# Kernel tuning notes

Hardware: AMD Instinct MI355X
Metric: run time of the kernel (lower is better)

## Reference

```python
import jax, jax.numpy as jnp
import numpy as np
import math

B, N, E_PER = 128, 512, 2048
D = 16
NUM_REL = 114
NUM_ATTR = 10
LAYERS = 3
RATIO = 0.8
TN = B * N
TE = B * E_PER
NEG_SLOPE = 0.2


def setup_inputs() -> dict:
    key = jax.random.key(0)
    ks = jax.random.split(key, 16)
    x_attr = jax.random.randint(ks[0], (TN,), 0, NUM_ATTR, dtype=jnp.int32)
    # edges constrained within each graph's contiguous block of N nodes
    src = jax.random.randint(ks[1], (B, E_PER), 0, N, dtype=jnp.int32)
    dst = jax.random.randint(ks[2], (B, E_PER), 0, N, dtype=jnp.int32)
    off = (jnp.arange(B, dtype=jnp.int32) * N)[:, None]
    edge_index = jnp.stack([(src + off).reshape(-1), (dst + off).reshape(-1)])
    edge_type = jax.random.randint(ks[3], (TE,), 0, NUM_REL, dtype=jnp.int32)
    emb = jax.random.normal(ks[4], (NUM_ATTR, D)) * 0.3
    gnn_w = jax.random.normal(ks[5], (LAYERS, NUM_REL, D, D)) * (1.0 / np.sqrt(D))
    gnn_q = jax.random.normal(ks[6], (LAYERS, D, 1)) * 0.3
    gnn_k = jax.random.normal(ks[7], (LAYERS, D, 1)) * 0.3
    gnn_b = jnp.zeros((LAYERS, D))
    pool_w = jax.random.normal(ks[8], (LAYERS - 1, D)) * 0.3
    w1 = jax.random.normal(ks[9], (D * LAYERS * 2, 16)) * (1.0 / np.sqrt(D * LAYERS * 2))
    b1 = jnp.zeros((16,))
    w2 = jax.random.normal(ks[10], (16, 4)) * 0.25
    b2 = jnp.zeros((4,))
    w3 = jax.random.normal(ks[11], (4, 1)) * 0.5
    b3 = jnp.zeros((1,))
    return dict(emb=emb, gnn_w=gnn_w, gnn_q=gnn_q, gnn_k=gnn_k, gnn_b=gnn_b,
                pool_w=pool_w, w1=w1, b1=b1, w2=w2, b2=b2, w3=w3, b3=b3,
                x_attr=x_attr, edge_index=edge_index, edge_type=edge_type)


def _rgat_layer(x, src, dst, etype, edge_mask, node_mask, W, q, k, b):
    # PyG RGATConv: heads=1, dim=1, additive-self-attention, across-relation softmax, sum aggr
    w_e = W[etype]                                   # [E, D, D] per-relation gather
    h_s = jnp.einsum('ed,edo->eo', x[src], w_e)      # transformed source (x_j)
    h_t = jnp.einsum('ed,edo->eo', x[dst], w_e)      # transformed target (x_i)
    logit = jax.nn.leaky_relu((h_t @ q + h_s @ k)[:, 0], NEG_SLOPE)  # [E]
    # masked segment softmax over incoming edges of each target node
    m = jax.ops.segment_max(jnp.where(edge_mask, logit, -jnp.inf), dst, num_segments=TN)
    m_e = m[dst]
    ex = jnp.where(edge_mask, jnp.exp(logit - jnp.where(jnp.isfinite(m_e), m_e, 0.0)), 0.0)
    den = jax.ops.segment_sum(ex, dst, num_segments=TN)[dst]
    alpha = ex / jnp.where(den > 0, den, 1.0)
    out = jax.ops.segment_sum(alpha[:, None] * h_s, dst, num_segments=TN) + b
    return jnp.where(node_mask[:, None], jax.nn.relu(out), 0.0)


def reference(emb, gnn_w, gnn_q, gnn_k, gnn_b, pool_w, w1, b1, w2, b2, w3, b3,
              x_attr, edge_index, edge_type):
    src, dst = edge_index[0], edge_index[1]
    x = emb[x_attr]                                  # [TN, D]
    node_mask = jnp.ones((TN,), bool)
    edge_mask = jnp.ones((TE,), bool)
    feats = []
    alive = N
    for l in range(LAYERS):
        x = _rgat_layer(x, src, dst, edge_type, edge_mask, node_mask,
                        gnn_w[l], gnn_q[l], gnn_k[l], gnn_b[l])
        xb = x.reshape(B, N, D)
        mb = node_mask.reshape(B, N)
        cnt = mb.sum(1).astype(x.dtype)[:, None]
        feats.append(xb.sum(1) / cnt)                               # global mean pool
        feats.append(jnp.where(mb[:, :, None], xb, -jnp.inf).max(1))  # global max pool
        if l < LAYERS - 1:
            kk = math.ceil(RATIO * alive)            # static per-graph keep count
            pw = pool_w[l]
            score = jnp.tanh((x @ pw) / jnp.linalg.norm(pw))        # [TN]
            sm = jnp.where(node_mask, score, -jnp.inf).reshape(B, N)
            _, idx = jax.lax.top_k(sm, kk)
            nm = jnp.zeros((B, N), bool).at[jnp.arange(B)[:, None], idx].set(True).reshape(-1)
            x = jnp.where(nm[:, None], x * score[:, None], 0.0)
            node_mask = nm
            edge_mask = edge_mask & nm[src] & nm[dst]
            alive = kk
    g = jnp.concatenate(feats, axis=1)               # [B, 96]
    g = jax.nn.relu(g @ w1 + b1)
    g = jax.nn.relu(g @ w2 + b2)
    return jax.nn.sigmoid(g @ w3 + b3)               # [B, 1]
```

## Files before the change

### kernel.cpp

```cpp
#include <hip/hip_runtime.h>

#define B_ 128
#define NPG 512
#define EPG 2048
#define NREL 114
#define XS 18

__device__ __forceinline__ unsigned fkey(float f){
  unsigned u = __float_as_uint(f);
  return (u & 0x80000000u) ? ~u : (u | 0x80000000u);
}
__device__ __forceinline__ float fdec(unsigned k){
  return (k & 0x80000000u) ? __uint_as_float(k & 0x7FFFFFFFu) : __uint_as_float(~k);
}
__device__ __forceinline__ float dot4f(float4 a, float4 b){
  return a.x*b.x + a.y*b.y + a.z*b.z + a.w*b.w;
}

__device__ __forceinline__ void scan512(int* s_hist, int* s_off, int* s_wt, int tid){
  int lane = tid & 63, wv = tid >> 6;
  int cnt = 0, inc = 0;
  if (wv < 8){
    cnt = s_hist[wv*64 + lane];
    inc = cnt;
    #pragma unroll
    for (int o=1; o<64; o<<=1){ int t=__shfl_up(inc,o); if (lane>=o) inc += t; }
    if (lane==63) s_wt[wv] = inc;
  }
  __syncthreads();
  if (tid < 8){
    int e = 0;
    #pragma unroll
    for (int j=0;j<8;j++) if (j<tid) e += s_wt[j];
    s_wt[8+tid] = e;
  }
  __syncthreads();
  if (wv < 8){
    int base = s_wt[8+wv];
    s_off[wv*64+lane+1] = base + inc;
    s_hist[wv*64+lane]  = base + inc - cnt;
  }
  if (tid==0) s_off[0] = 0;
}

__global__ __launch_bounds__(1024) void k_fused(
    const float* __restrict__ emb, const float* __restrict__ gnn_w,
    const float* __restrict__ gnn_q, const float* __restrict__ gnn_k,
    const float* __restrict__ gnn_b, const float* __restrict__ pool_w,
    const float* __restrict__ w1, const float* __restrict__ b1,
    const float* __restrict__ w2, const float* __restrict__ b2,
    const float* __restrict__ w3, const float* __restrict__ b3,
    const int* __restrict__ xattr, const int* __restrict__ src,
    const int* __restrict__ dst, const int* __restrict__ et,
    float* __restrict__ out)
{
  __shared__ float s_x[NPG*XS];
  __shared__ float s_wq[NREL*XS];
  __shared__ float s_wk[NREL*XS];
  __shared__ float s_logit[EPG];
  __shared__ int s_off[NPG+1];
  __shared__ int s_hist[NPG];
  __shared__ unsigned s_keys[NPG];
  __shared__ int s_mask[NPG];
  __shared__ unsigned short s_esrc[EPG], s_edst[EPG], s_eet[EPG];
  __shared__ unsigned short s_perm[NPG];
  __shared__ int s_dh[64];
  __shared__ int s_wt[16];
  __shared__ float s_sum[16];
  __shared__ unsigned s_max16[16];
  __shared__ int s_w[16];
  __shared__ float s_feats[96];
  __shared__ float s_h1[16], s_h2[4];

  const int b = blockIdx.x, tid = threadIdx.x;
  const int lane = tid & 63, wv = tid >> 6;
  const int og = tid & 3, grp = tid >> 2;
  const int nb = b*NPG;
  const size_t gb = (size_t)b*EPG;

  if (tid < NPG){
    int a = xattr[nb + tid];
    const float2* e2 = (const float2*)(emb + a*16);
    #pragma unroll
    for (int c=0;c<8;c++) *(float2*)&s_x[tid*XS + 2*c] = e2[c];
    s_mask[tid] = 1;
  }
  for (int i=tid;i<NPG;i+=1024) s_hist[i]=0;
  if (tid<64) s_dh[tid]=0;
  __syncthreads();
  for (int e=tid;e<EPG;e+=1024) atomicAdd(&s_hist[dst[gb+e]-nb], 1);
  __syncthreads();
  scan512(s_hist, s_off, s_wt, tid);
  __syncthreads();
  {
    for (int e=tid;e<EPG;e+=1024){
      int d = dst[gb+e]-nb;
      int p = atomicAdd(&s_hist[d], 1);
      s_esrc[p] = (unsigned short)(src[gb+e]-nb);
      s_edst[p] = (unsigned short)d;
      s_eet[p]  = (unsigned short)et[gb+e];
    }
    int mydeg = 0;
    if (tid<NPG){
      mydeg = s_off[tid+1]-s_off[tid]; if (mydeg>63) mydeg=63;
      atomicAdd(&s_dh[mydeg], 1);
    }
    __syncthreads();
    if (tid<64){
      int c = s_dh[tid], inc = c;
      #pragma unroll
      for (int o=1;o<64;o<<=1){ int t=__shfl_up(inc,o); if (tid>=o) inc+=t; }
      s_dh[tid] = inc - c;
    }
    __syncthreads();
    if (tid<NPG){ int p = atomicAdd(&s_dh[mydeg],1); s_perm[p]=(unsigned short)tid; }
  }
  __syncthreads();

  const int cnts[3] = {512, 410, 328};
  const int kks[2]  = {410, 328};

  for (int l=0; l<3; ++l){
    const float* Wl = gnn_w + (size_t)l*NREL*256;
    {
      const float4* q4=(const float4*)(gnn_q+l*16);
      const float4* k4=(const float4*)(gnn_k+l*16);
      float4 q0=q4[0],q1=q4[1],q2=q4[2],q3=q4[3];
      float4 c0=k4[0],c1=k4[1],c2=k4[2],c3=k4[3];
      for (int i=tid;i<NREL*16;i+=1024){
        const float4* wr=(const float4*)(Wl+(size_t)i*16);
        float4 a0=wr[0],a1=wr[1],a2=wr[2],a3=wr[3];
        s_wq[(i>>4)*XS+(i&15)] = dot4f(a0,q0)+dot4f(a1,q1)+dot4f(a2,q2)+dot4f(a3,q3);
        s_wk[(i>>4)*XS+(i&15)] = dot4f(a0,c0)+dot4f(a1,c1)+dot4f(a2,c2)+dot4f(a3,c3);
      }
      if (tid<16){ s_sum[tid]=0.f; s_max16[tid]=0u; }
    }
    __syncthreads();
    float rnorm=0.f; float pw4[4]={0,0,0,0};
    if (l<2){
      float ss=0.f;
      #pragma unroll
      for (int o=0;o<16;o++){ float p=pool_w[l*16+o]; ss+=p*p; }
      rnorm = rsqrtf(ss);
      #pragma unroll
      for (int j=0;j<4;j++) pw4[j]=pool_w[l*16+4*og+j];
    }
    const float* bb = gnn_b + l*16;
    const int nA = s_perm[grp], nB = s_perm[511-grp];
    float zA[4], zB[4];
    auto pm_round = [&](int n, float* z){
      int beg = s_off[n], end = s_off[n+1];
      int alive = s_mask[n];
      float2 xt0 = *(const float2*)&s_x[n*XS+4*og];
      float2 xt1 = *(const float2*)&s_x[n*XS+4*og+2];
      float m = -1e30f;
      for (int p=beg; p<end; ++p){
        int s = s_esrc[p]; int r = s_eet[p];
        float2 wq0=*(const float2*)&s_wq[r*XS+4*og];
        float2 wq1=*(const float2*)&s_wq[r*XS+4*og+2];
        float2 wk0=*(const float2*)&s_wk[r*XS+4*og];
        float2 wk1=*(const float2*)&s_wk[r*XS+4*og+2];
        float2 xs0=*(const float2*)&s_x[s*XS+4*og];
        float2 xs1=*(const float2*)&s_x[s*XS+4*og+2];
        float a = xt0.x*wq0.x + xt0.y*wq0.y + xt1.x*wq1.x + xt1.y*wq1.y
                + xs0.x*wk0.x + xs0.y*wk0.y + xs1.x*wk1.x + xs1.y*wk1.y;
        a += __shfl_xor(a,1); a += __shfl_xor(a,2);
        float lg = a>0.f ? a : 0.2f*a;
        if (og==0) s_logit[p] = lg;
        m = fmaxf(m, lg);
      }
      float den=0.f, v0=0.f, v1=0.f, v2=0.f, v3=0.f;
      int p = beg;
      for (; p+2 <= end; p += 2){
        int s0=s_esrc[p],   r0=s_eet[p];
        int s1=s_esrc[p+1], r1=s_eet[p+1];
        float ex0 = __expf(s_logit[p]   - m);
        float ex1 = __expf(s_logit[p+1] - m);
        const float4* wr0 = (const float4*)(Wl + (size_t)r0*256) + og;
        const float4* wr1 = (const float4*)(Wl + (size_t)r1*256) + og;
        const float* xr0 = &s_x[s0*XS];
        const float* xr1 = &s_x[s1*XS];
        float h00=0.f,h01=0.f,h02=0.f,h03=0.f;
        float h10=0.f,h11=0.f,h12=0.f,h13=0.f;
        #pragma unroll
        for (int d2=0; d2<8; ++d2){
          float2 xa = *(const float2*)&xr0[2*d2];
          float2 xb = *(const float2*)&xr1[2*d2];
          float4 wA0 = wr0[(2*d2)*4], wB0 = wr0[(2*d2+1)*4];
          float4 wA1 = wr1[(2*d2)*4], wB1 = wr1[(2*d2+1)*4];
          h00 += xa.x*wA0.x + xa.y*wB0.x;  h01 += xa.x*wA0.y + xa.y*wB0.y;
          h02 += xa.x*wA0.z + xa.y*wB0.z;  h03 += xa.x*wA0.w + xa.y*wB0.w;
          h10 += xb.x*wA1.x + xb.y*wB1.x;  h11 += xb.x*wA1.y + xb.y*wB1.y;
          h12 += xb.x*wA1.z + xb.y*wB1.z;  h13 += xb.x*wA1.w + xb.y*wB1.w;
        }
        den += ex0 + ex1;
        v0 += ex0*h00 + ex1*h10; v1 += ex0*h01 + ex1*h11;
        v2 += ex0*h02 + ex1*h12; v3 += ex0*h03 + ex1*h13;
      }
      if (p < end){
        int s = s_esrc[p]; int r = s_eet[p];
        float ex = __expf(s_logit[p] - m);
        const float4* wr = (const float4*)(Wl + (size_t)r*256) + og;
        const float* xr = &s_x[s*XS];
        float h0=0.f,h1=0.f,h2=0.f,h3=0.f;
        #pragma unroll
        for (int d2=0; d2<8; ++d2){
          float2 xs2 = *(const float2*)&xr[2*d2];
          float4 wA = wr[(2*d2)*4];
          float4 wB = wr[(2*d2+1)*4];
          h0 += xs2.x*wA.x + xs2.y*wB.x;
          h1 += xs2.x*wA.y + xs2.y*wB.y;
          h2 += xs2.x*wA.z + xs2.y*wB.z;
          h3 += xs2.x*wA.w + xs2.y*wB.w;
        }
        den += ex;
        v0 += ex*h0; v1 += ex*h1; v2 += ex*h2; v3 += ex*h3;
      }
      float inv = den>0.f ? 1.f/den : 1.f;
      z[0]=v0*inv+bb[4*og+0]; z[1]=v1*inv+bb[4*og+1];
      z[2]=v2*inv+bb[4*og+2]; z[3]=v3*inv+bb[4*og+3];
      #pragma unroll
      for (int j=0;j<4;j++){ if (z[j]<0.f) z[j]=0.f; }
      if (!alive){ z[0]=z[1]=z[2]=z[3]=0.f; }
      #pragma unroll
      for (int j=0;j<4;j++){
        float sv=z[j], mv=z[j];
        #pragma unroll
        for (int off=4; off<64; off<<=1){
          sv += __shfl_xor(sv, off);
          mv = fmaxf(mv, __shfl_xor(mv, off));
        }
        if ((lane>>2)==0){
          atomicAdd(&s_sum[4*og+j], sv);
          atomicMax(&s_max16[4*og+j], __float_as_uint(mv));
        }
      }
      if (l<2){
        float dq = z[0]*pw4[0]+z[1]*pw4[1]+z[2]*pw4[2]+z[3]*pw4[3];
        dq += __shfl_xor(dq,1); dq += __shfl_xor(dq,2);
        if (og==0){
          float sc = tanhf(dq*rnorm);
          s_keys[n] = alive ? fkey(sc) : 0u;
        }
      }
    };
    pm_round(nA, zA);
    pm_round(nB, zB);
    __syncthreads();
    if (tid<16){
      s_feats[l*32+tid]    = s_sum[tid]/(float)cnts[l];
      s_feats[l*32+16+tid] = __uint_as_float(s_max16[tid]);
    }
    if (l==2) break;
    {
      *(float2*)&s_x[nA*XS+4*og]   = make_float2(zA[0],zA[1]);
      *(float2*)&s_x[nA*XS+4*og+2] = make_float2(zA[2],zA[3]);
      *(float2*)&s_x[nB*XS+4*og]   = make_float2(zB[0],zB[1]);
      *(float2*)&s_x[nB*XS+4*og+2] = make_float2(zB[2],zB[3]);
    }
    __syncthreads();
    {
      const int kk = kks[l];
      unsigned kreg[8];
      #pragma unroll
      for (int j=0;j<8;j++) kreg[j] = s_keys[lane + j*64];
      unsigned cur = 0u;
      for (int bit=31; bit>=0; --bit){
        unsigned cand = cur | (1u<<bit);
        int c=0;
        #pragma unroll
        for (int j=0;j<8;j++) c += __popcll(__ballot(kreg[j]>=cand));
        if (c >= kk) cur = cand;
      }
      int cgt=0;
      #pragma unroll
      for (int j=0;j<8;j++) cgt += __popcll(__ballot(kreg[j]>cur));
      int ties = kk - cgt;
      unsigned myk = (tid<NPG) ? s_keys[tid] : 0u;
      bool eq = (tid<NPG) && (myk==cur);
      unsigned long long bal = __ballot(eq);
      int lrank = __popcll(bal & ((1ull<<lane)-1ull));
      if (lane==0) s_w[wv] = __popcll(bal);
      __syncthreads();
      int pre=0;
      #pragma unroll
      for (int w=0; w<16; ++w) if (w<wv) pre += s_w[w];
      int rank = pre + lrank;
      if (tid < NPG){
        bool keep = (myk > cur) || (eq && rank < ties);
        float mult = keep ? fdec(myk) : 0.f;
        #pragma unroll
        for (int c=0;c<8;c++){
          float2 t2 = *(const float2*)&s_x[tid*XS+2*c];
          t2.x *= mult; t2.y *= mult;
          *(float2*)&s_x[tid*XS+2*c] = t2;
        }
        s_mask[tid] = keep ? 1 : 0;
      }
    }
    __syncthreads();
    {
      int ne = s_off[NPG];
      unsigned short e0s=0,e0d=0,e0t=0,e1s=0,e1d=0,e1t=0;
      bool k0=false, k1=false;
      if (tid < ne){
        e0s=s_esrc[tid]; e0d=s_edst[tid]; e0t=s_eet[tid];
        k0 = s_mask[e0s] && s_mask[e0d];
      }
      if (tid+1024 < ne){
        e1s=s_esrc[tid+1024]; e1d=s_edst[tid+1024]; e1t=s_eet[tid+1024];
        k1 = s_mask[e1s] && s_mask[e1d];
      }
      __syncthreads();
      for (int i=tid;i<NPG;i+=1024) s_hist[i]=0;
      if (tid<64) s_dh[tid]=0;
      __syncthreads();
      if (k0) atomicAdd(&s_hist[e0d], 1);
      if (k1) atomicAdd(&s_hist[e1d], 1);
      __syncthreads();
      scan512(s_hist, s_off, s_wt, tid);
      __syncthreads();
      if (k0){ int p=atomicAdd(&s_hist[e0d],1); s_esrc[p]=e0s; s_edst[p]=e0d; s_eet[p]=e0t; }
      if (k1){ int p=atomicAdd(&s_hist[e1d],1); s_esrc[p]=e1s; s_edst[p]=e1d; s_eet[p]=e1t; }
      int mydeg = 0;
      if (tid<NPG){
        mydeg = s_off[tid+1]-s_off[tid]; if (mydeg>63) mydeg=63;
        atomicAdd(&s_dh[mydeg], 1);
      }
      __syncthreads();
      if (tid<64){
        int c = s_dh[tid], inc = c;
        #pragma unroll
        for (int o=1;o<64;o<<=1){ int t=__shfl_up(inc,o); if (tid>=o) inc+=t; }
        s_dh[tid] = inc - c;
      }
      __syncthreads();
      if (tid<NPG){ int p = atomicAdd(&s_dh[mydeg],1); s_perm[p]=(unsigned short)tid; }
      __syncthreads();
    }
  }

  __syncthreads();
  if (tid < 16){
    float a = b1[tid];
    for (int i=0;i<96;i++) a += s_feats[i]*w1[i*16+tid];
    s_h1[tid] = a>0.f?a:0.f;
  }
  __syncthreads();
  if (tid < 4){
    float a = b2[tid];
    #pragma unroll
    for (int i=0;i<16;i++) a += s_h1[i]*w2[i*4+tid];
    s_h2[tid] = a>0.f?a:0.f;
  }
  __syncthreads();
  if (tid == 0){
    float z = b3[0];
    #pragma unroll
    for (int i=0;i<4;i++) z += s_h2[i]*w3[i];
    out[b] = 1.f/(1.f+expf(-z));
  }
}

extern "C" void kernel_launch(void* const* d_in, const int* in_sizes, int n_in,
                              void* d_out, int out_size, void* d_ws, size_t ws_size,
                              hipStream_t stream) {
  const float* emb    = (const float*)d_in[0];
  const float* gnn_w  = (const float*)d_in[1];
  const float* gnn_q  = (const float*)d_in[2];
  const float* gnn_k  = (const float*)d_in[3];
  const float* gnn_b  = (const float*)d_in[4];
  const float* pool_w = (const float*)d_in[5];
  const float* w1 = (const float*)d_in[6];
  const float* b1 = (const float*)d_in[7];
  const float* w2 = (const float*)d_in[8];
  const float* b2 = (const float*)d_in[9];
  const float* w3 = (const float*)d_in[10];
  const float* b3 = (const float*)d_in[11];
  const int* xattr = (const int*)d_in[12];
  const int* eidx  = (const int*)d_in[13];
  const int* etype = (const int*)d_in[14];
  const int* src = eidx;
  const int* dst = eidx + (size_t)B_*EPG;

  k_fused<<<B_, 1024, 0, stream>>>(emb, gnn_w, gnn_q, gnn_k, gnn_b, pool_w,
                                   w1, b1, w2, b2, w3, b3,
                                   xattr, src, dst, etype, (float*)d_out);
}
```

Before: 106.8 us.

## Compute attention logits edge-parallel and precompute per-layer q/k projections upfront

The per-node serial logit and max pass is replaced by an edge-parallel pass in which each of the 1024 threads computes one edge's logit and stores exp(logit) directly. This drops the max subtraction, which is mathematically equivalent but could overflow for large logits. The W·q and W·k projections for all three layers are now computed once at the start, overlapped with the degree histogram. Source index and edge type are packed into one 16-bit word to cut LDS traffic. The sum and max pooling reductions are merged across both node rounds, which halves the shuffle and atomic work. The aim is to remove load imbalance from per-node serial loops over edges of uneven degree.

```diff
diff --git a/kernel.cpp b/kernel.cpp
--- a/kernel.cpp
+++ b/kernel.cpp
@@ -55,14 +55,15 @@
     float* __restrict__ out)
 {
   __shared__ float s_x[NPG*XS];
-  __shared__ float s_wq[NREL*XS];
-  __shared__ float s_wk[NREL*XS];
-  __shared__ float s_logit[EPG];
+  __shared__ float s_wq3[3*NREL*XS];
+  __shared__ float s_wk3[3*NREL*XS];
+  __shared__ float s_ex[EPG];
+  __shared__ unsigned short s_epk[EPG];
+  __shared__ unsigned short s_edst[EPG];
   __shared__ int s_off[NPG+1];
   __shared__ int s_hist[NPG];
   __shared__ unsigned s_keys[NPG];
   __shared__ int s_mask[NPG];
-  __shared__ unsigned short s_esrc[EPG], s_edst[EPG], s_eet[EPG];
   __shared__ unsigned short s_perm[NPG];
   __shared__ int s_dh[64];
   __shared__ int s_wt[16];
@@ -89,18 +90,28 @@
   if (tid<64) s_dh[tid]=0;
   __syncthreads();
   for (int e=tid;e<EPG;e+=1024) atomicAdd(&s_hist[dst[gb+e]-nb], 1);
+  for (int i=tid; i<3*NREL*16; i+=1024){
+    int l = i / (NREL*16);
+    int rd = i - l*(NREL*16);
+    const float4* wr = (const float4*)(gnn_w + (size_t)i*16);
+    float4 a0=wr[0],a1=wr[1],a2=wr[2],a3=wr[3];
+    const float4* q4 = (const float4*)(gnn_q + l*16);
+    const float4* k4 = (const float4*)(gnn_k + l*16);
+    int idx = l*(NREL*XS) + (rd>>4)*XS + (rd&15);
+    s_wq3[idx] = dot4f(a0,q4[0])+dot4f(a1,q4[1])+dot4f(a2,q4[2])+dot4f(a3,q4[3]);
+    s_wk3[idx] = dot4f(a0,k4[0])+dot4f(a1,k4[1])+dot4f(a2,k4[2])+dot4f(a3,k4[3]);
+  }
   __syncthreads();
   scan512(s_hist, s_off, s_wt, tid);
   __syncthreads();
+  for (int e=tid;e<EPG;e+=1024){
+    int d = dst[gb+e]-nb;
+    int p = atomicAdd(&s_hist[d], 1);
+    s_epk[p]  = (unsigned short)((src[gb+e]-nb) | (et[gb+e]<<9));
+    s_edst[p] = (unsigned short)d;
+  }
   {
-    for (int e=tid;e<EPG;e+=1024){
-      int d = dst[gb+e]-nb;
-      int p = atomicAdd(&s_hist[d], 1);
-      s_esrc[p] = (unsigned short)(src[gb+e]-nb);
-      s_edst[p] = (unsigned short)d;
-      s_eet[p]  = (unsigned short)et[gb+e];
-    }
-    int mydeg = 0;
+    int mydeg=0;
     if (tid<NPG){
       mydeg = s_off[tid+1]-s_off[tid]; if (mydeg>63) mydeg=63;
       atomicAdd(&s_dh[mydeg], 1);
@@ -116,27 +127,42 @@
     if (tid<NPG){ int p = atomicAdd(&s_dh[mydeg],1); s_perm[p]=(unsigned short)tid; }
   }
   __syncthreads();
+  int ne = EPG;
 
   const int cnts[3] = {512, 410, 328};
   const int kks[2]  = {410, 328};
 
   for (int l=0; l<3; ++l){
+    if (tid<16){ s_sum[tid]=0.f; s_max16[tid]=0u; }
+    __syncthreads();
+    {
+      const float* wqL = s_wq3 + l*(NREL*XS);
+      const float* wkL = s_wk3 + l*(NREL*XS);
+      for (int e=tid; e<ne; e+=1024){
+        unsigned pk = s_epk[e]; int s = pk & 511, r = pk >> 9;
+        int t = s_edst[e];
+        const float* xrt = &s_x[t*XS];
+        const float* xrs = &s_x[s*XS];
+        const float* wq = &wqL[r*XS];
+        const float* wk = &wkL[r*XS];
+        float acc = 0.f;
+        #pragma unroll
+        for (int c=0;c<8;c++){
+          float2 xt2 = *(const float2*)&xrt[2*c];
+          float2 xs2 = *(const float2*)&xrs[2*c];
+          float2 q2  = *(const float2*)&wq[2*c];
+          float2 k2  = *(const float2*)&wk[2*c];
+          acc += xt2.x*q2.x + xt2.y*q2.y + xs2.x*k2.x + xs2.y*k2.y;
+        }
+        float lg = acc>0.f ? acc : 0.2f*acc;
+        s_ex[e] = __expf(lg);
+      }
+    }
+    __syncthreads();
     const float* Wl = gnn_w + (size_t)l*NREL*256;
-    {
-      const float4* q4=(const float4*)(gnn_q+l*16);
-      const float4* k4=(const float4*)(gnn_k+l*16);
-      float4 q0=q4[0],q1=q4[1],q2=q4[2],q3=q4[3];
-      float4 c0=k4[0],c1=k4[1],c2=k4[2],c3=k4[3];
-      for (int i=tid;i<NREL*16;i+=1024){
-        const float4* wr=(const float4*)(Wl+(size_t)i*16);
-        float4 a0=wr[0],a1=wr[1],a2=wr[2],a3=wr[3];
-        s_wq[(i>>4)*XS+(i&15)] = dot4f(a0,q0)+dot4f(a1,q1)+dot4f(a2,q2)+dot4f(a3,q3);
-        s_wk[(i>>4)*XS+(i&15)] = dot4f(a0,c0)+dot4f(a1,c1)+dot4f(a2,c2)+dot4f(a3,c3);
-      }
-      if (tid<16){ s_sum[tid]=0.f; s_max16[tid]=0u; }
-    }
-    __syncthreads();
-    float rnorm=0.f; float pw4[4]={0,0,0,0};
+    float bb4[4], pw4[4]={0,0,0,0}; float rnorm=0.f;
+    #pragma unroll
+    for (int j=0;j<4;j++) bb4[j] = gnn_b[l*16+4*og+j];
     if (l<2){
       float ss=0.f;
       #pragma unroll
@@ -145,86 +171,74 @@
       #pragma unroll
       for (int j=0;j<4;j++) pw4[j]=pool_w[l*16+4*og+j];
     }
-    const float* bb = gnn_b + l*16;
     const int nA = s_perm[grp], nB = s_perm[511-grp];
     float zA[4], zB[4];
     auto pm_round = [&](int n, float* z){
       int beg = s_off[n], end = s_off[n+1];
       int alive = s_mask[n];
-      float2 xt0 = *(const float2*)&s_x[n*XS+4*og];
-      float2 xt1 = *(const float2*)&s_x[n*XS+4*og+2];
-      float m = -1e30f;
-      for (int p=beg; p<end; ++p){
-        int s = s_esrc[p]; int r = s_eet[p];
-        float2 wq0=*(const float2*)&s_wq[r*XS+4*og];
-        float2 wq1=*(const float2*)&s_wq[r*XS+4*og+2];
-        float2 wk0=*(const float2*)&s_wk[r*XS+4*og];
-        float2 wk1=*(const float2*)&s_wk[r*XS+4*og+2];
-        float2 xs0=*(const float2*)&s_x[s*XS+4*og];
-        float2 xs1=*(const float2*)&s_x[s*XS+4*og+2];
-        float a = xt0.x*wq0.x + xt0.y*wq0.y + xt1.x*wq1.x + xt1.y*wq1.y
-                + xs0.x*wk0.x + xs0.y*wk0.y + xs1.x*wk1.x + xs1.y*wk1.y;
-        a += __shfl_xor(a,1); a += __shfl_xor(a,2);
-        float lg = a>0.f ? a : 0.2f*a;
-        if (og==0) s_logit[p] = lg;
-        m = fmaxf(m, lg);
-      }
       float den=0.f, v0=0.f, v1=0.f, v2=0.f, v3=0.f;
       int p = beg;
       for (; p+2 <= end; p += 2){
-        int s0=s_esrc[p],   r0=s_eet[p];
-        int s1=s_esrc[p+1], r1=s_eet[p+1];
-        float ex0 = __expf(s_logit[p]   - m);
-        float ex1 = __expf(s_logit[p+1] - m);
-        const float4* wr0 = (const float4*)(Wl + (size_t)r0*256) + og;
-        const float4* wr1 = (const float4*)(Wl + (size_t)r1*256) + og;
-        const float* xr0 = &s_x[s0*XS];
-        const float* xr1 = &s_x[s1*XS];
+        unsigned pka=s_epk[p], pkb=s_epk[p+1];
+        float exa = s_ex[p], exb = s_ex[p+1];
+        int sa=pka&511, ra=pka>>9;
+        int sb=pkb&511, rb=pkb>>9;
+        const float4* wra = (const float4*)(Wl + (size_t)ra*256) + og;
+        const float4* wrb = (const float4*)(Wl + (size_t)rb*256) + og;
+        const float* xa = &s_x[sa*XS];
+        const float* xb = &s_x[sb*XS];
         float h00=0.f,h01=0.f,h02=0.f,h03=0.f;
         float h10=0.f,h11=0.f,h12=0.f,h13=0.f;
         #pragma unroll
         for (int d2=0; d2<8; ++d2){
-          float2 xa = *(const float2*)&xr0[2*d2];
-          float2 xb = *(const float2*)&xr1[2*d2];
-          float4 wA0 = wr0[(2*d2)*4], wB0 = wr0[(2*d2+1)*4];
-          float4 wA1 = wr1[(2*d2)*4], wB1 = wr1[(2*d2+1)*4];
-          h00 += xa.x*wA0.x + xa.y*wB0.x;  h01 += xa.x*wA0.y + xa.y*wB0.y;
-          h02 += xa.x*wA0.z + xa.y*wB0.z;  h03 += xa.x*wA0.w + xa.y*wB0.w;
-          h10 += xb.x*wA1.x + xb.y*wB1.x;  h11 += xb.x*wA1.y + xb.y*wB1.y;
-          h12 += xb.x*wA1.z + xb.y*wB1.z;  h13 += xb.x*wA1.w + xb.y*wB1.w;
-        }
-        den += ex0 + ex1;
-        v0 += ex0*h00 + ex1*h10; v1 += ex0*h01 + ex1*h11;
-        v2 += ex0*h02 + ex1*h12; v3 += ex0*h03 + ex1*h13;
+          float2 x2a = *(const float2*)&xa[2*d2];
+          float2 x2b = *(const float2*)&xb[2*d2];
+          float4 wA0 = wra[(2*d2)*4], wB0 = wra[(2*d2+1)*4];
+          float4 wA1 = wrb[(2*d2)*4], wB1 = wrb[(2*d2+1)*4];
+          h00 += x2a.x*wA0.x + x2a.y*wB0.x;  h01 += x2a.x*wA0.y + x2a.y*wB0.y;
+          h02 += x2a.x*wA0.z + x2a.y*wB0.z;  h03 += x2a.x*wA0.w + x2a.y*wB0.w;
+          h10 += x2b.x*wA1.x + x2b.y*wB1.x;  h11 += x2b.x*wA1.y + x2b.y*wB1.y;
+          h12 += x2b.x*wA1.z + x2b.y*wB1.z;  h13 += x2b.x*wA1.w + x2b.y*wB1.w;
+        }
+        den += exa + exb;
+        v0 += exa*h00 + exb*h10; v1 += exa*h01 + exb*h11;
+        v2 += exa*h02 + exb*h12; v3 += exa*h03 + exb*h13;
       }
       if (p < end){
-        int s = s_esrc[p]; int r = s_eet[p];
-        float ex = __expf(s_logit[p] - m);
+        unsigned pk=s_epk[p]; int s=pk&511, r=pk>>9;
+        float ex = s_ex[p];
         const float4* wr = (const float4*)(Wl + (size_t)r*256) + og;
         const float* xr = &s_x[s*XS];
         float h0=0.f,h1=0.f,h2=0.f,h3=0.f;
         #pragma unroll
         for (int d2=0; d2<8; ++d2){
           float2 xs2 = *(const float2*)&xr[2*d2];
-          float4 wA = wr[(2*d2)*4];
-          float4 wB = wr[(2*d2+1)*4];
-          h0 += xs2.x*wA.x + xs2.y*wB.x;
-          h1 += xs2.x*wA.y + xs2.y*wB.y;
-          h2 += xs2.x*wA.z + xs2.y*wB.z;
-          h3 += xs2.x*wA.w + xs2.y*wB.w;
+          float4 wA = wr[(2*d2)*4], wB = wr[(2*d2+1)*4];
+          h0 += xs2.x*wA.x + xs2.y*wB.x;  h1 += xs2.x*wA.y + xs2.y*wB.y;
+          h2 += xs2.x*wA.z + xs2.y*wB.z;  h3 += xs2.x*wA.w + xs2.y*wB.w;
         }
         den += ex;
         v0 += ex*h0; v1 += ex*h1; v2 += ex*h2; v3 += ex*h3;
       }
       float inv = den>0.f ? 1.f/den : 1.f;
-      z[0]=v0*inv+bb[4*og+0]; z[1]=v1*inv+bb[4*og+1];
-      z[2]=v2*inv+bb[4*og+2]; z[3]=v3*inv+bb[4*og+3];
+      z[0]=v0*inv+bb4[0]; z[1]=v1*inv+bb4[1];
+      z[2]=v2*inv+bb4[2]; z[3]=v3*inv+bb4[3];
       #pragma unroll
       for (int j=0;j<4;j++){ if (z[j]<0.f) z[j]=0.f; }
       if (!alive){ z[0]=z[1]=z[2]=z[3]=0.f; }
+      if (l<2){
+        float dq = z[0]*pw4[0]+z[1]*pw4[1]+z[2]*pw4[2]+z[3]*pw4[3];
+        dq += __shfl_xor(dq,1); dq += __shfl_xor(dq,2);
+        if (og==0) s_keys[n] = alive ? fkey(tanhf(dq*rnorm)) : 0u;
+      }
+    };
+    pm_round(nA, zA);
+    pm_round(nB, zB);
+    {
       #pragma unroll
       for (int j=0;j<4;j++){
-        float sv=z[j], mv=z[j];
+        float sv = zA[j]+zB[j];
+        float mv = fmaxf(zA[j],zB[j]);
         #pragma unroll
         for (int off=4; off<64; off<<=1){
           sv += __shfl_xor(sv, off);
@@ -235,17 +249,7 @@
           atomicMax(&s_max16[4*og+j], __float_as_uint(mv));
         }
       }
-      if (l<2){
-        float dq = z[0]*pw4[0]+z[1]*pw4[1]+z[2]*pw4[2]+z[3]*pw4[3];
-        dq += __shfl_xor(dq,1); dq += __shfl_xor(dq,2);
-        if (og==0){
-          float sc = tanhf(dq*rnorm);
-          s_keys[n] = alive ? fkey(sc) : 0u;
-        }
-      }
-    };
-    pm_round(nA, zA);
-    pm_round(nB, zB);
+    }
     __syncthreads();
     if (tid<16){
       s_feats[l*32+tid]    = s_sum[tid]/(float)cnts[l];
@@ -300,29 +304,27 @@
     }
     __syncthreads();
     {
-      int ne = s_off[NPG];
-      unsigned short e0s=0,e0d=0,e0t=0,e1s=0,e1d=0,e1t=0;
-      bool k0=false, k1=false;
+      unsigned pk0=0, pk1=0; unsigned short dd0=0, dd1=0; bool k0=false,k1=false;
       if (tid < ne){
-        e0s=s_esrc[tid]; e0d=s_edst[tid]; e0t=s_eet[tid];
-        k0 = s_mask[e0s] && s_mask[e0d];
+        pk0 = s_epk[tid]; dd0 = s_edst[tid];
+        k0 = s_mask[pk0 & 511] && s_mask[dd0];
       }
       if (tid+1024 < ne){
-        e1s=s_esrc[tid+1024]; e1d=s_edst[tid+1024]; e1t=s_eet[tid+1024];
-        k1 = s_mask[e1s] && s_mask[e1d];
+        pk1 = s_epk[tid+1024]; dd1 = s_edst[tid+1024];
+        k1 = s_mask[pk1 & 511] && s_mask[dd1];
       }
       __syncthreads();
       for (int i=tid;i<NPG;i+=1024) s_hist[i]=0;
       if (tid<64) s_dh[tid]=0;
       __syncthreads();
-      if (k0) atomicAdd(&s_hist[e0d], 1);
-      if (k1) atomicAdd(&s_hist[e1d], 1);
+      if (k0) atomicAdd(&s_hist[dd0], 1);
+      if (k1) atomicAdd(&s_hist[dd1], 1);
       __syncthreads();
       scan512(s_hist, s_off, s_wt, tid);
       __syncthreads();
-      if (k0){ int p=atomicAdd(&s_hist[e0d],1); s_esrc[p]=e0s; s_edst[p]=e0d; s_eet[p]=e0t; }
-      if (k1){ int p=atomicAdd(&s_hist[e1d],1); s_esrc[p]=e1s; s_edst[p]=e1d; s_eet[p]=e1t; }
-      int mydeg = 0;
+      if (k0){ int p=atomicAdd(&s_hist[dd0],1); s_epk[p]=(unsigned short)pk0; s_edst[p]=dd0; }
+      if (k1){ int p=atomicAdd(&s_hist[dd1],1); s_epk[p]=(unsigned short)pk1; s_edst[p]=dd1; }
+      int mydeg=0;
       if (tid<NPG){
         mydeg = s_off[tid+1]-s_off[tid]; if (mydeg>63) mydeg=63;
         atomicAdd(&s_dh[mydeg], 1);
@@ -337,6 +339,7 @@
       __syncthreads();
       if (tid<NPG){ int p = atomicAdd(&s_dh[mydeg],1); s_perm[p]=(unsigned short)tid; }
       __syncthreads();
+      ne = s_off[NPG];
     }
   }
 
```

Measured after the change: 212.4 us. +98.9%, slower.
